# Optimization experiments

Hardware: AMD Instinct MI355X
Metric: run time of the kernel (lower is better)

Reference implementation:

```python
import jax, jax.numpy as jnp
import numpy as np

D_MODEL = 768
D_FF = 3072
N_EXPERTS = 9  # num_experts + 1 (expert 0 is the common expert)


def setup_inputs() -> dict:
    key = jax.random.key(0)
    ks = jax.random.split(key, 7)
    scale = 0.02
    return {
        "x": jax.random.normal(ks[0], (2, 1024, D_MODEL), jnp.float32),
        "Ws": jax.random.normal(ks[1], (D_MODEL, N_EXPERTS), jnp.float32) * scale,
        "bs": jnp.zeros((N_EXPERTS,), jnp.float32),
        "W1": jax.random.normal(ks[2], (N_EXPERTS, D_MODEL, D_FF), jnp.float32) * scale,
        "b1": jnp.zeros((N_EXPERTS, D_FF), jnp.float32),
        "W2": jax.random.normal(ks[3], (N_EXPERTS, D_FF, D_MODEL), jnp.float32) * scale,
        "b2": jnp.zeros((N_EXPERTS, D_MODEL), jnp.float32),
    }


def reference(x, Ws, bs, W1, b1, W2, b2):
    B, S, d = x.shape
    xt = x.reshape(-1, d)  # [T, d]
    # top-1 switch router
    route_prob = jax.nn.softmax(xt @ Ws + bs, axis=-1)  # [T, E]
    p = jnp.max(route_prob, axis=-1)       # [T]
    routes = jnp.argmax(route_prob, axis=-1)  # [T]
    # dense grouped FFN: every expert on every token (reference baseline)
    h = jax.nn.gelu(jnp.einsum('td,edf->tef', xt, W1) + b1, approximate=False)  # [T, E, f]
    out = jnp.einsum('tef,efd->ted', h, W2) + b2  # [T, E, d]
    common = out[:, 0, :]  # common expert output for all tokens
    sel = jnp.take_along_axis(out, routes[:, None, None], axis=1)[:, 0, :]  # [T, d]
    # tokens routed to expert 0: common * (p / stop_grad(p))  (==common in fwd)
    scaling = (p / jax.lax.stop_gradient(p))[:, None]
    pe = p[:, None]
    final = jnp.where((routes == 0)[:, None],
                      common * scaling,
                      pe * sel + (1.0 - pe) * common)
    return final.reshape(B, S, d)
```

## Files before the change

### kernel.cpp

```cpp
#include <hip/hip_runtime.h>
#include <stdint.h>
#include <math.h>

#define T_TOK 2048
#define DM 768
#define DF 3072
#define NE 9

typedef unsigned short ushort_t;
typedef __attribute__((ext_vector_type(8))) __bf16 bf16x8;
typedef __attribute__((ext_vector_type(4))) float f32x4;

__device__ __forceinline__ unsigned short f2bf(float f) {
  union { float f; uint32_t u; } v; v.f = f;
  uint32_t u = v.u;
  u = u + 0x7fffu + ((u >> 16) & 1u);
  return (unsigned short)(u >> 16);
}

__device__ __forceinline__ void gl_lds16(const void* g, void* l) {
  __builtin_amdgcn_global_load_lds(
      (const __attribute__((address_space(1))) unsigned int*)g,
      (__attribute__((address_space(3))) unsigned int*)l, 16, 0, 0);
}

__global__ __launch_bounds__(256) void route_kernel(
    const float* __restrict__ x, const float* __restrict__ Ws,
    const float* __restrict__ bs, ushort_t* __restrict__ xb,
    float* __restrict__ p, int* __restrict__ routes,
    int* __restrict__ counts, int* __restrict__ lists) {
  const int wave = threadIdx.x >> 6, lane = threadIdx.x & 63;
  const int t = blockIdx.x * 4 + wave;
  const float* xr = x + (size_t)t * DM;
  const int d0 = lane * 12;
  float xv[12];
#pragma unroll
  for (int i = 0; i < 12; ++i) xv[i] = xr[d0 + i];
#pragma unroll
  for (int i = 0; i < 3; ++i) {
    ushort4 s;
    s.x = f2bf(xv[i * 4 + 0]); s.y = f2bf(xv[i * 4 + 1]);
    s.z = f2bf(xv[i * 4 + 2]); s.w = f2bf(xv[i * 4 + 3]);
    *(ushort4*)(xb + (size_t)t * DM + d0 + i * 4) = s;
  }
  float acc[NE];
#pragma unroll
  for (int e = 0; e < NE; ++e) acc[e] = 0.f;
#pragma unroll
  for (int i = 0; i < 12; ++i) {
    const float* wr = Ws + (size_t)(d0 + i) * NE;
#pragma unroll
    for (int e = 0; e < NE; ++e) acc[e] += xv[i] * wr[e];
  }
#pragma unroll
  for (int off = 32; off >= 1; off >>= 1)
#pragma unroll
    for (int e = 0; e < NE; ++e) acc[e] += __shfl_xor(acc[e], off);
  if (lane == 0) {
    float m = -1e30f; int am = 0;
#pragma unroll
    for (int e = 0; e < NE; ++e) {
      float l = acc[e] + bs[e];
      acc[e] = l;
      if (l > m) { m = l; am = e; }
    }
    float s = 0.f;
#pragma unroll
    for (int e = 0; e < NE; ++e) s += expf(acc[e] - m);
    p[t] = 1.0f / s;
    routes[t] = am;
    if (am != 0) {
      int pos = atomicAdd(&counts[am], 1);
      lists[(am - 1) * T_TOK + pos] = t;
    }
  }
}

__global__ __launch_bounds__(256) void transpose_conv(
    const float* __restrict__ in, ushort_t* __restrict__ out,
    int R, int C) {
  __shared__ float tile[64][65];
  const int e = blockIdx.z;
  const float* src = in + (size_t)e * R * C;
  ushort_t* dst = out + (size_t)e * R * C;
  const int c0 = blockIdx.x * 64, r0 = blockIdx.y * 64;
  const int k = threadIdx.x & 15, g = threadIdx.x >> 4;
#pragma unroll
  for (int i = 0; i < 4; ++i) {
    const float4 v =
        *(const float4*)(src + (size_t)(r0 + g + i * 16) * C + c0 + k * 4);
    tile[g + i * 16][k * 4 + 0] = v.x;
    tile[g + i * 16][k * 4 + 1] = v.y;
    tile[g + i * 16][k * 4 + 2] = v.z;
    tile[g + i * 16][k * 4 + 3] = v.w;
  }
  __syncthreads();
#pragma unroll
  for (int i = 0; i < 4; ++i) {
    const int c = g + i * 16;
    ushort4 s;
    s.x = f2bf(tile[k * 4 + 0][c]);
    s.y = f2bf(tile[k * 4 + 1][c]);
    s.z = f2bf(tile[k * 4 + 2][c]);
    s.w = f2bf(tile[k * 4 + 3][c]);
    *(ushort4*)(dst + (size_t)(c0 + c) * R + r0 + k * 4) = s;
  }
}

template <int K, int N, int BM, bool PASS1>
__global__ __launch_bounds__(256) void ffn_gemm(
    const ushort_t* __restrict__ Asrc0, const ushort_t* __restrict__ AsrcS,
    const ushort_t* __restrict__ Btb, const float* __restrict__ bias,
    const int* __restrict__ counts, const int* __restrict__ lists,
    ushort_t* __restrict__ D0b, ushort_t* __restrict__ DSb,
    float* __restrict__ D0f, float* __restrict__ DSf) {
  constexpr int GX = T_TOK / BM;
  constexpr int GY = N / 128;
  constexpr int P = GY * NE;
  const unsigned r = blockIdx.x;
  const int c = r & 7u;
  const unsigned j = r >> 3;
  const int i = j / GX;
  const int k = j % GX;
  const int pid = c + 8 * i;
  if (pid >= P) return;
  const int by = pid % GY;
  const int e = pid / GY;

  const int cnt = (e == 0) ? T_TOK : counts[e];
  const int m0 = k * BM;
  if (m0 >= cnt) return;
  const int n0 = by * 128;
  const int* list = lists + (e - 1) * T_TOK;
  const ushort_t* Asrc = (e == 0) ? Asrc0 : AsrcS;

  __shared__ ushort_t As[BM * 64];
  __shared__ ushort_t Bs[128 * 64];

  const int tid = threadIdx.x;
  const int wave = tid >> 6, lane = tid & 63;
  const int g = lane >> 4, lr = lane & 15;
  constexpr int AI = BM / 32;
  constexpr int MR = BM / 32;

  const ushort_t* Bbase = Btb + ((size_t)e * N + n0) * K;

  const ushort_t* aSrcPtr[AI];
  const ushort_t* bSrcPtr[4];
#pragma unroll
  for (int ii = 0; ii < AI; ++ii) {
    int cidx = (wave * AI + ii) * 64 + lane;
    int row = cidx >> 3;
    int ch = (cidx & 7) ^ (row & 7);
    int mrow = m0 + row;
    int tok = (e == 0) ? mrow : list[mrow < cnt ? mrow : cnt - 1];
    aSrcPtr[ii] = Asrc + (size_t)tok * K + ch * 8;
  }
#pragma unroll
  for (int ii = 0; ii < 4; ++ii) {
    int cidx = (wave * 4 + ii) * 64 + lane;
    int row = cidx >> 3;
    int ch = (cidx & 7) ^ (row & 7);
    bSrcPtr[ii] = Bbase + (size_t)row * K + ch * 8;
  }

  f32x4 acc[MR][4];
#pragma unroll
  for (int mi = 0; mi < MR; ++mi)
#pragma unroll
    for (int ni = 0; ni < 4; ++ni) acc[mi][ni] = (f32x4){0.f, 0.f, 0.f, 0.f};

  const int wm = wave >> 1, wn = wave & 1;
  const int swz = (lr & 7) << 4;

  for (int k0 = 0; k0 < K; k0 += 64) {
#pragma unroll
    for (int ii = 0; ii < AI; ++ii)
      gl_lds16(aSrcPtr[ii] + k0, &As[(wave * AI + ii) * 512]);
#pragma unroll
    for (int ii = 0; ii < 4; ++ii)
      gl_lds16(bSrcPtr[ii] + k0, &Bs[(wave * 4 + ii) * 512]);
    __syncthreads();
#pragma unroll
    for (int kk = 0; kk < 2; ++kk) {
      bf16x8 af[MR], bfv[4];
#pragma unroll
      for (int mi = 0; mi < MR; ++mi) {
        int row = wm * (MR * 16) + mi * 16 + lr;
        int off = row * 128 + ((kk * 64 + g * 16) ^ swz);
        af[mi] = *(const bf16x8*)((const char*)As + off);
      }
#pragma unroll
      for (int ni = 0; ni < 4; ++ni) {
        int row = wn * 64 + ni * 16 + lr;
        int off = row * 128 + ((kk * 64 + g * 16) ^ swz);
        bfv[ni] = *(const bf16x8*)((const char*)Bs + off);
      }
#pragma unroll
      for (int mi = 0; mi < MR; ++mi)
#pragma unroll
        for (int ni = 0; ni < 4; ++ni)
          acc[mi][ni] = __builtin_amdgcn_mfma_f32_16x16x32_bf16(
              af[mi], bfv[ni], acc[mi][ni], 0, 0, 0);
    }
    __syncthreads();
  }

#pragma unroll
  for (int mi = 0; mi < MR; ++mi) {
#pragma unroll
    for (int rr = 0; rr < 4; ++rr) {
      const int mrow = m0 + wm * (MR * 16) + mi * 16 + g * 4 + rr;
      if (mrow >= cnt) continue;
      const int tok = (e == 0) ? mrow : list[mrow];
#pragma unroll
      for (int ni = 0; ni < 4; ++ni) {
        const int col = n0 + wn * 64 + ni * 16 + lr;
        float v = acc[mi][ni][rr] + bias[e * N + col];
        if constexpr (PASS1) {
          float gv = 0.5f * v * (1.0f + erff(v * 0.70710678118654752f));
          ushort_t* Dst = (e == 0) ? D0b : DSb;
          Dst[(size_t)tok * N + col] = f2bf(gv);
        } else {
          float* Dst = (e == 0) ? D0f : DSf;
          Dst[(size_t)tok * N + col] = v;
        }
      }
    }
  }
}

__global__ __launch_bounds__(256) void combine_kernel(
    const float* __restrict__ Ocm, const float* __restrict__ Osel,
    const float* __restrict__ p, const int* __restrict__ routes,
    float* __restrict__ out) {
  const int idx = blockIdx.x * blockDim.x + threadIdx.x;
  const int t = idx / (DM / 4);
  f32x4 cm = ((const f32x4*)Ocm)[idx];
  const int r = routes[t];
  f32x4 res;
  if (r == 0) {
    res = cm;
  } else {
    const float pe = p[t];
    f32x4 sl = ((const f32x4*)Osel)[idx];
    res = pe * sl + (1.0f - pe) * cm;
  }
  ((f32x4*)out)[idx] = res;
}

extern "C" void kernel_launch(void* const* d_in, const int* in_sizes, int n_in,
                              void* d_out, int out_size, void* d_ws,
                              size_t ws_size, hipStream_t stream) {
  const float* x  = (const float*)d_in[0];
  const float* Ws = (const float*)d_in[1];
  const float* bs = (const float*)d_in[2];
  const float* W1 = (const float*)d_in[3];
  const float* b1 = (const float*)d_in[4];
  const float* W2 = (const float*)d_in[5];
  const float* b2 = (const float*)d_in[6];
  float* out = (float*)d_out;
  char* ws = (char*)d_ws;

  constexpr size_t XB_OFF  = 0;
  constexpr size_t WTB_OFF = XB_OFF + (size_t)T_TOK * DM * 2;
  constexpr size_t H0_OFF  = WTB_OFF + (size_t)NE * DF * DM * 2;
  constexpr size_t HS_OFF  = H0_OFF + (size_t)T_TOK * DF * 2;
  constexpr size_t OC_OFF  = HS_OFF + (size_t)T_TOK * DF * 2;
  constexpr size_t OS_OFF  = OC_OFF + (size_t)T_TOK * DM * 4;
  constexpr size_t P_OFF   = OS_OFF + (size_t)T_TOK * DM * 4;
  constexpr size_t RT_OFF  = P_OFF + (size_t)T_TOK * 4;
  constexpr size_t CNT_OFF = RT_OFF + (size_t)T_TOK * 4;
  constexpr size_t LST_OFF = CNT_OFF + 64;

  ushort_t* xb   = (ushort_t*)(ws + XB_OFF);
  ushort_t* Wtb  = (ushort_t*)(ws + WTB_OFF);
  ushort_t* H0   = (ushort_t*)(ws + H0_OFF);
  ushort_t* Hsel = (ushort_t*)(ws + HS_OFF);
  float* Ocm     = (float*)(ws + OC_OFF);
  float* Osel    = (float*)(ws + OS_OFF);
  float* p       = (float*)(ws + P_OFF);
  int* routes    = (int*)(ws + RT_OFF);
  int* counts    = (int*)(ws + CNT_OFF);
  int* lists     = (int*)(ws + LST_OFF);

  hipMemsetAsync(counts, 0, 64, stream);
  route_kernel<<<T_TOK / 4, 256, 0, stream>>>(x, Ws, bs, xb, p, routes, counts,
                                              lists);
  transpose_conv<<<dim3(DF / 64, DM / 64, NE), 256, 0, stream>>>(W1, Wtb, DM,
                                                                 DF);
  {
    constexpr int GX = T_TOK / 128, P = (DF / 128) * NE;
    constexpr int nblk = GX * 8 * ((P + 7) / 8);
    ffn_gemm<DM, DF, 128, true><<<nblk, 256, 0, stream>>>(
        xb, xb, Wtb, b1, counts, lists, H0, Hsel, nullptr, nullptr);
  }
  transpose_conv<<<dim3(DM / 64, DF / 64, NE), 256, 0, stream>>>(W2, Wtb, DF,
                                                                 DM);
  {
    constexpr int GX = T_TOK / 64, P = (DM / 128) * NE;
    constexpr int nblk = GX * 8 * ((P + 7) / 8);
    ffn_gemm<DF, DM, 64, false><<<nblk, 256, 0, stream>>>(
        H0, Hsel, Wtb, b2, counts, lists, nullptr, nullptr, Ocm, Osel);
  }
  combine_kernel<<<(T_TOK * DM / 4) / 256, 256, 0, stream>>>(Ocm, Osel, p,
                                                             routes, out);
}
```

Before: 392.2 us.

## Split-K second FFN GEMM, 3D grid launch, fold bias into combine

```diff
diff --git a/kernel.cpp b/kernel.cpp
--- a/kernel.cpp
+++ b/kernel.cpp
@@ -107,30 +107,20 @@
   }
 }
 
-template <int K, int N, int BM, bool PASS1>
+template <int K, int N, int BM, bool PASS1, int KSPLIT>
 __global__ __launch_bounds__(256) void ffn_gemm(
     const ushort_t* __restrict__ Asrc0, const ushort_t* __restrict__ AsrcS,
     const ushort_t* __restrict__ Btb, const float* __restrict__ bias,
     const int* __restrict__ counts, const int* __restrict__ lists,
     ushort_t* __restrict__ D0b, ushort_t* __restrict__ DSb,
     float* __restrict__ D0f, float* __restrict__ DSf) {
-  constexpr int GX = T_TOK / BM;
-  constexpr int GY = N / 128;
-  constexpr int P = GY * NE;
-  const unsigned r = blockIdx.x;
-  const int c = r & 7u;
-  const unsigned j = r >> 3;
-  const int i = j / GX;
-  const int k = j % GX;
-  const int pid = c + 8 * i;
-  if (pid >= P) return;
-  const int by = pid % GY;
-  const int e = pid / GY;
-
+  const int zid = blockIdx.z;
+  const int e = zid % NE;
+  const int kc = zid / NE;
   const int cnt = (e == 0) ? T_TOK : counts[e];
-  const int m0 = k * BM;
+  const int m0 = blockIdx.x * BM;
   if (m0 >= cnt) return;
-  const int n0 = by * 128;
+  const int n0 = blockIdx.y * 128;
   const int* list = lists + (e - 1) * T_TOK;
   const ushort_t* Asrc = (e == 0) ? Asrc0 : AsrcS;
 
@@ -142,6 +132,7 @@
   const int g = lane >> 4, lr = lane & 15;
   constexpr int AI = BM / 32;
   constexpr int MR = BM / 32;
+  constexpr int KC = K / KSPLIT;
 
   const ushort_t* Bbase = Btb + ((size_t)e * N + n0) * K;
 
@@ -173,7 +164,7 @@
   const int wm = wave >> 1, wn = wave & 1;
   const int swz = (lr & 7) << 4;
 
-  for (int k0 = 0; k0 < K; k0 += 64) {
+  for (int k0 = kc * KC; k0 < (kc + 1) * KC; k0 += 64) {
 #pragma unroll
     for (int ii = 0; ii < AI; ++ii)
       gl_lds16(aSrcPtr[ii] + k0, &As[(wave * AI + ii) * 512]);
@@ -216,14 +207,14 @@
 #pragma unroll
       for (int ni = 0; ni < 4; ++ni) {
         const int col = n0 + wn * 64 + ni * 16 + lr;
-        float v = acc[mi][ni][rr] + bias[e * N + col];
         if constexpr (PASS1) {
+          float v = acc[mi][ni][rr] + bias[e * N + col];
           float gv = 0.5f * v * (1.0f + erff(v * 0.70710678118654752f));
           ushort_t* Dst = (e == 0) ? D0b : DSb;
           Dst[(size_t)tok * N + col] = f2bf(gv);
         } else {
-          float* Dst = (e == 0) ? D0f : DSf;
-          Dst[(size_t)tok * N + col] = v;
+          float* Dst = ((e == 0) ? D0f : DSf) + (size_t)kc * T_TOK * N;
+          Dst[(size_t)tok * N + col] = acc[mi][ni][rr];
         }
       }
     }
@@ -231,19 +222,24 @@
 }
 
 __global__ __launch_bounds__(256) void combine_kernel(
-    const float* __restrict__ Ocm, const float* __restrict__ Osel,
-    const float* __restrict__ p, const int* __restrict__ routes,
-    float* __restrict__ out) {
+    const float* __restrict__ Pc, const float* __restrict__ Ps,
+    const float* __restrict__ b2, const float* __restrict__ p,
+    const int* __restrict__ routes, float* __restrict__ out) {
   const int idx = blockIdx.x * blockDim.x + threadIdx.x;
   const int t = idx / (DM / 4);
-  f32x4 cm = ((const f32x4*)Ocm)[idx];
+  const int col4 = (idx % (DM / 4)) * 4;
+  f32x4 cm = ((const f32x4*)Pc)[idx];
+  cm += ((const f32x4*)(Pc + (size_t)T_TOK * DM))[idx];
+  cm += *(const f32x4*)(b2 + col4);
   const int r = routes[t];
   f32x4 res;
   if (r == 0) {
     res = cm;
   } else {
     const float pe = p[t];
-    f32x4 sl = ((const f32x4*)Osel)[idx];
+    f32x4 sl = ((const f32x4*)Ps)[idx];
+    sl += ((const f32x4*)(Ps + (size_t)T_TOK * DM))[idx];
+    sl += *(const f32x4*)(b2 + (size_t)r * DM + col4);
     res = pe * sl + (1.0f - pe) * cm;
   }
   ((f32x4*)out)[idx] = res;
@@ -266,9 +262,9 @@
   constexpr size_t WTB_OFF = XB_OFF + (size_t)T_TOK * DM * 2;
   constexpr size_t H0_OFF  = WTB_OFF + (size_t)NE * DF * DM * 2;
   constexpr size_t HS_OFF  = H0_OFF + (size_t)T_TOK * DF * 2;
-  constexpr size_t OC_OFF  = HS_OFF + (size_t)T_TOK * DF * 2;
-  constexpr size_t OS_OFF  = OC_OFF + (size_t)T_TOK * DM * 4;
-  constexpr size_t P_OFF   = OS_OFF + (size_t)T_TOK * DM * 4;
+  constexpr size_t PC_OFF  = HS_OFF + (size_t)T_TOK * DF * 2;
+  constexpr size_t PS_OFF  = PC_OFF + (size_t)2 * T_TOK * DM * 4;
+  constexpr size_t P_OFF   = PS_OFF + (size_t)2 * T_TOK * DM * 4;
   constexpr size_t RT_OFF  = P_OFF + (size_t)T_TOK * 4;
   constexpr size_t CNT_OFF = RT_OFF + (size_t)T_TOK * 4;
   constexpr size_t LST_OFF = CNT_OFF + 64;
@@ -277,8 +273,8 @@
   ushort_t* Wtb  = (ushort_t*)(ws + WTB_OFF);
   ushort_t* H0   = (ushort_t*)(ws + H0_OFF);
   ushort_t* Hsel = (ushort_t*)(ws + HS_OFF);
-  float* Ocm     = (float*)(ws + OC_OFF);
-  float* Osel    = (float*)(ws + OS_OFF);
+  float* Pc      = (float*)(ws + PC_OFF);
+  float* Psel    = (float*)(ws + PS_OFF);
   float* p       = (float*)(ws + P_OFF);
   int* routes    = (int*)(ws + RT_OFF);
   int* counts    = (int*)(ws + CNT_OFF);
@@ -289,20 +285,14 @@
                                               lists);
   transpose_conv<<<dim3(DF / 64, DM / 64, NE), 256, 0, stream>>>(W1, Wtb, DM,
                                                                  DF);
-  {
-    constexpr int GX = T_TOK / 128, P = (DF / 128) * NE;
-    constexpr int nblk = GX * 8 * ((P + 7) / 8);
-    ffn_gemm<DM, DF, 128, true><<<nblk, 256, 0, stream>>>(
-        xb, xb, Wtb, b1, counts, lists, H0, Hsel, nullptr, nullptr);
-  }
+  ffn_gemm<DM, DF, 64, true, 1>
+      <<<dim3(T_TOK / 64, DF / 128, NE), 256, 0, stream>>>(
+          xb, xb, Wtb, b1, counts, lists, H0, Hsel, nullptr, nullptr);
   transpose_conv<<<dim3(DM / 64, DF / 64, NE), 256, 0, stream>>>(W2, Wtb, DF,
                                                                  DM);
-  {
-    constexpr int GX = T_TOK / 64, P = (DM / 128) * NE;
-    constexpr int nblk = GX * 8 * ((P + 7) / 8);
-    ffn_gemm<DF, DM, 64, false><<<nblk, 256, 0, stream>>>(
-        H0, Hsel, Wtb, b2, counts, lists, nullptr, nullptr, Ocm, Osel);
-  }
-  combine_kernel<<<(T_TOK * DM / 4) / 256, 256, 0, stream>>>(Ocm, Osel, p,
+  ffn_gemm<DF, DM, 64, false, 2>
+      <<<dim3(T_TOK / 64, DM / 128, NE * 2), 256, 0, stream>>>(
+          H0, Hsel, Wtb, nullptr, counts, lists, nullptr, nullptr, Pc, Psel);
+  combine_kernel<<<(T_TOK * DM / 4) / 256, 256, 0, stream>>>(Pc, Psel, b2, p,
                                                              routes, out);
 }
```

Result: slower. 496.4 us (+26.6%).
